# Optimization experiments

Measured on AMD Instinct MI355X. Metric: run time of the kernel, lower is better.

## Reference

```python
import jax, jax.numpy as jnp
import numpy as np

N, E, D = 50000, 300000, 64
EPS = 0.0  # eps buffer, train_eps=False


def setup_inputs() -> dict:
    key = jax.random.key(0)
    ks = jax.random.split(key, 24)
    inp = {}
    i = 0
    for d in range(3):
        inp[f"x{d}"] = jax.random.normal(ks[i], (N, D), jnp.float32); i += 1
        inp[f"up_index{d}"] = jax.random.randint(ks[i], (2, E), 0, N, jnp.int32); i += 1
        inp[f"down_index{d}"] = jax.random.randint(ks[i], (2, E), 0, N, jnp.int32); i += 1
        inp[f"up_attr{d}"] = jax.random.normal(ks[i], (E, D), jnp.float32); i += 1
        inp[f"down_attr{d}"] = jax.random.normal(ks[i], (E, D), jnp.float32); i += 1
    s2 = 1.0 / np.sqrt(2 * D)
    s1 = 1.0 / np.sqrt(D)
    inp["W_up"] = jax.random.normal(ks[i], (2 * D, D), jnp.float32) * s2; i += 1
    inp["b_up"] = jnp.zeros((D,), jnp.float32)
    inp["W_down"] = jax.random.normal(ks[i], (2 * D, D), jnp.float32) * s2; i += 1
    inp["b_down"] = jnp.zeros((D,), jnp.float32)
    inp["W1"] = jax.random.normal(ks[i], (D, D), jnp.float32) * s1; i += 1
    inp["b1"] = jnp.zeros((D,), jnp.float32)
    inp["W2"] = jax.random.normal(ks[i], (D, D), jnp.float32) * s1; i += 1
    inp["b2"] = jnp.zeros((D,), jnp.float32)
    return inp


def _level(x, up_idx, down_idx, up_attr, down_attr,
           W_up, b_up, W_down, b_down, W1, b1, W2, b2):
    # message_up: gather source feats, concat attr, MLP, scatter-add to targets
    m_up = jax.nn.relu(jnp.concatenate([x[up_idx[1]], up_attr], axis=-1) @ W_up + b_up)
    out_up = jax.ops.segment_sum(m_up, up_idx[0], num_segments=N)
    m_dn = jax.nn.relu(jnp.concatenate([x[down_idx[1]], down_attr], axis=-1) @ W_down + b_down)
    out_dn = jax.ops.segment_sum(m_dn, down_idx[0], num_segments=N)
    # out_up += (1+eps)x; out_down += (1+eps)x; update(out_up + out_down)
    h = out_up + out_dn + (2.0 * (1.0 + EPS)) * x
    return jax.nn.relu(jax.nn.relu(h @ W1 + b1) @ W2 + b2)


def reference(x0, up_index0, down_index0, up_attr0, down_attr0,
              x1, up_index1, down_index1, up_attr1, down_attr1,
              x2, up_index2, down_index2, up_attr2, down_attr2,
              W_up, b_up, W_down, b_down, W1, b1, W2, b2):
    params = (W_up, b_up, W_down, b_down, W1, b1, W2, b2)
    o0 = _level(x0, up_index0, down_index0, up_attr0, down_attr0, *params)
    o1 = _level(x1, up_index1, down_index1, up_attr1, down_attr1, *params)
    o2 = _level(x2, up_index2, down_index2, up_attr2, down_attr2, *params)
    return (o0, o1, o2)
```

## Files before the change

kernel.cpp:

```cpp
#include <hip/hip_runtime.h>
#include <hip/hip_fp16.h>

#define NN 50000
#define NE 300000
#define ETILES (NE / 16)
#define NTILES (NN / 16)

typedef _Float16 f16;
typedef _Float16 f16x4 __attribute__((ext_vector_type(4)));
typedef float f32x4 __attribute__((ext_vector_type(4)));

__device__ __forceinline__ f16x4 cvt4(float4 v) {
    f16x4 r; r.x = (f16)v.x; r.y = (f16)v.y; r.z = (f16)v.z; r.w = (f16)v.w;
    return r;
}

template<bool HALF>
__global__ void init_kernel(const float* __restrict__ x0, const float* __restrict__ x1,
                            const float* __restrict__ x2, void* __restrict__ hbase) {
    const size_t i = (size_t)blockIdx.x * 256 + threadIdx.x;
    const int lvl = (int)(i / (NN * 16));
    const size_t li = i - (size_t)lvl * (NN * 16);
    const float* xs = (lvl == 0) ? x0 : (lvl == 1) ? x1 : x2;
    float4 v = ((const float4*)xs)[li];
    if (HALF) {
        f16x4 o;
        o.x = (f16)(2.f * v.x); o.y = (f16)(2.f * v.y);
        o.z = (f16)(2.f * v.z); o.w = (f16)(2.f * v.w);
        ((f16x4*)((f16*)hbase + (size_t)lvl * NN * 64))[li] = o;
    } else {
        ((float4*)((float*)hbase + (size_t)lvl * NN * 64))[li] =
            make_float4(2.f * v.x, 2.f * v.y, 2.f * v.z, 2.f * v.w);
    }
}

template<bool HALF>
__global__ __launch_bounds__(256) void edge_kernel(
    const float* __restrict__ x, const int* __restrict__ idx,
    const float* __restrict__ attr, const float* __restrict__ W,
    const float* __restrict__ b, void* __restrict__ hv) {

    const int t    = threadIdx.x;
    const int lane = t & 63;
    const int wid  = t >> 6;
    const int lr   = lane & 15;
    const int lg   = (lane >> 4) & 3;

    f16x4 wf[8][4];
#pragma unroll
    for (int k0 = 0; k0 < 8; ++k0) {
        const int kb = k0 * 16 + 4 * lg;
#pragma unroll
        for (int n = 0; n < 4; ++n) {
            const int c = n * 16 + lr;
            f16x4 w;
            w.x = (f16)W[(kb + 0) * 64 + c];
            w.y = (f16)W[(kb + 1) * 64 + c];
            w.z = (f16)W[(kb + 2) * 64 + c];
            w.w = (f16)W[(kb + 3) * 64 + c];
            wf[k0][n] = w;
        }
    }
    float bf[4];
#pragma unroll
    for (int n = 0; n < 4; ++n) bf[n] = b[n * 16 + lr];

    const float4* x4 = (const float4*)x;
    const float4* a4 = (const float4*)attr;

    const int gw     = blockIdx.x * 4 + wid;
    const int stride = gridDim.x * 4;
    for (int tile = gw; tile < ETILES; tile += stride) {
        const int e0  = tile << 4;
        const int src = idx[NE + e0 + lr];
        int tg[4];
#pragma unroll
        for (int j = 0; j < 4; ++j) tg[j] = idx[e0 + 4 * lg + j];

        f16x4 a[8];
#pragma unroll
        for (int k0 = 0; k0 < 4; ++k0)
            a[k0] = cvt4(x4[(size_t)src * 16 + 4 * k0 + lg]);
#pragma unroll
        for (int k0 = 0; k0 < 4; ++k0)
            a[4 + k0] = cvt4(a4[(size_t)(e0 + lr) * 16 + 4 * k0 + lg]);

        f32x4 acc[4];
#pragma unroll
        for (int n = 0; n < 4; ++n) acc[n] = (f32x4){0.f, 0.f, 0.f, 0.f};
#pragma unroll
        for (int k0 = 0; k0 < 8; ++k0) {
#pragma unroll
            for (int n = 0; n < 4; ++n)
                acc[n] = __builtin_amdgcn_mfma_f32_16x16x16f16(a[k0], wf[k0][n], acc[n], 0, 0, 0);
        }

#pragma unroll
        for (int j = 0; j < 4; ++j) {
            float v[4], vn[4];
#pragma unroll
            for (int n = 0; n < 4; ++n) v[n] = fmaxf(acc[n][j] + bf[n], 0.f);
#pragma unroll
            for (int n = 0; n < 4; ++n) vn[n] = __shfl_xor(v[n], 1);
            if (HALF) {
                __half* hp = (__half*)hv + (size_t)tg[j] * 64;
                if ((lane & 1) == 0) {
                    unsafeAtomicAdd((__half2*)(hp + 0 * 16 + lr), __floats2half2_rn(v[0], vn[0]));
                    unsafeAtomicAdd((__half2*)(hp + 1 * 16 + lr), __floats2half2_rn(v[1], vn[1]));
                } else {
                    unsafeAtomicAdd((__half2*)(hp + 2 * 16 + lr - 1), __floats2half2_rn(vn[2], v[2]));
                    unsafeAtomicAdd((__half2*)(hp + 3 * 16 + lr - 1), __floats2half2_rn(vn[3], v[3]));
                }
            } else {
                float* hp = (float*)hv + (size_t)tg[j] * 64;
#pragma unroll
                for (int n = 0; n < 4; ++n)
                    unsafeAtomicAdd(hp + n * 16 + lr, v[n]);
            }
        }
    }
}

template<bool HALF>
__global__ __launch_bounds__(256) void node_kernel(
    const void* __restrict__ hbase, float* __restrict__ outb,
    const float* __restrict__ W1, const float* __restrict__ b1,
    const float* __restrict__ W2, const float* __restrict__ b2) {

    __shared__ f16 Y[4][16 * 72];

    const int t    = threadIdx.x;
    const int lane = t & 63;
    const int wid  = t >> 6;
    const int lr   = lane & 15;
    const int lg   = (lane >> 4) & 3;

    f16x4 w1f[4][4], w2f[4][4];
#pragma unroll
    for (int k0 = 0; k0 < 4; ++k0) {
        const int kb = k0 * 16 + 4 * lg;
#pragma unroll
        for (int n = 0; n < 4; ++n) {
            const int c = n * 16 + lr;
            f16x4 w;
            w.x = (f16)W1[(kb + 0) * 64 + c];
            w.y = (f16)W1[(kb + 1) * 64 + c];
            w.z = (f16)W1[(kb + 2) * 64 + c];
            w.w = (f16)W1[(kb + 3) * 64 + c];
            w1f[k0][n] = w;
            w.x = (f16)W2[(kb + 0) * 64 + c];
            w.y = (f16)W2[(kb + 1) * 64 + c];
            w.z = (f16)W2[(kb + 2) * 64 + c];
            w.w = (f16)W2[(kb + 3) * 64 + c];
            w2f[k0][n] = w;
        }
    }
    float b1f[4], b2f[4];
#pragma unroll
    for (int n = 0; n < 4; ++n) {
        b1f[n] = b1[n * 16 + lr];
        b2f[n] = b2[n * 16 + lr];
    }

    const int gw     = blockIdx.x * 4 + wid;
    const int stride = gridDim.x * 4;
    for (int tile = gw; tile < 3 * NTILES; tile += stride) {
        const int lvl = tile / NTILES;
        const int n0  = (tile - lvl * NTILES) << 4;
        float* out = outb + (size_t)lvl * NN * 64;

        f16x4 a[4];
        if (HALF) {
            const f16* h16 = (const f16*)hbase + (size_t)lvl * NN * 64;
#pragma unroll
            for (int k0 = 0; k0 < 4; ++k0)
                a[k0] = *(const f16x4*)&h16[(size_t)(n0 + lr) * 64 + k0 * 16 + 4 * lg];
        } else {
            const float4* h4 = (const float4*)((const float*)hbase + (size_t)lvl * NN * 64);
#pragma unroll
            for (int k0 = 0; k0 < 4; ++k0)
                a[k0] = cvt4(h4[(size_t)(n0 + lr) * 16 + 4 * k0 + lg]);
        }

        f32x4 acc[4];
#pragma unroll
        for (int n = 0; n < 4; ++n) acc[n] = (f32x4){0.f, 0.f, 0.f, 0.f};
#pragma unroll
        for (int k0 = 0; k0 < 4; ++k0)
#pragma unroll
            for (int n = 0; n < 4; ++n)
                acc[n] = __builtin_amdgcn_mfma_f32_16x16x16f16(a[k0], w1f[k0][n], acc[n], 0, 0, 0);

#pragma unroll
        for (int n = 0; n < 4; ++n)
#pragma unroll
            for (int j = 0; j < 4; ++j) {
                float v = acc[n][j] + b1f[n];
                v = v > 0.f ? v : 0.f;
                Y[wid][(4 * lg + j) * 72 + n * 16 + lr] = (f16)v;
            }

        f16x4 a2[4];
#pragma unroll
        for (int k0 = 0; k0 < 4; ++k0)
            a2[k0] = *(const f16x4*)&Y[wid][lr * 72 + k0 * 16 + 4 * lg];

        f32x4 acc2[4];
#pragma unroll
        for (int n = 0; n < 4; ++n) acc2[n] = (f32x4){0.f, 0.f, 0.f, 0.f};
#pragma unroll
        for (int k0 = 0; k0 < 4; ++k0)
#pragma unroll
            for (int n = 0; n < 4; ++n)
                acc2[n] = __builtin_amdgcn_mfma_f32_16x16x16f16(a2[k0], w2f[k0][n], acc2[n], 0, 0, 0);

#pragma unroll
        for (int n = 0; n < 4; ++n)
#pragma unroll
            for (int j = 0; j < 4; ++j) {
                float v = acc2[n][j] + b2f[n];
                v = v > 0.f ? v : 0.f;
                out[(size_t)(n0 + 4 * lg + j) * 64 + n * 16 + lr] = v;
            }
    }
}

extern "C" void kernel_launch(void* const* d_in, const int* in_sizes, int n_in,
                              void* d_out, int out_size, void* d_ws, size_t ws_size,
                              hipStream_t stream) {
    (void)in_sizes; (void)n_in; (void)out_size;

    const float* W_up   = (const float*)d_in[15];
    const float* b_up   = (const float*)d_in[16];
    const float* W_down = (const float*)d_in[17];
    const float* b_down = (const float*)d_in[18];
    const float* W1     = (const float*)d_in[19];
    const float* b1     = (const float*)d_in[20];
    const float* W2     = (const float*)d_in[21];
    const float* b2     = (const float*)d_in[22];

    const float* x0 = (const float*)d_in[0];
    const float* x1 = (const float*)d_in[5];
    const float* x2 = (const float*)d_in[10];

    const bool half_ok = ws_size >= (size_t)3 * NN * 64 * sizeof(__half);

    if (half_ok) {
        f16* hbase = (f16*)d_ws;
        init_kernel<true><<<9375, 256, 0, stream>>>(x0, x1, x2, hbase);
        for (int d = 0; d < 3; ++d) {
            const float* x  = (const float*)d_in[5 * d + 0];
            const int*   ui = (const int*)  d_in[5 * d + 1];
            const int*   di = (const int*)  d_in[5 * d + 2];
            const float* ua = (const float*)d_in[5 * d + 3];
            const float* da = (const float*)d_in[5 * d + 4];
            void* h = hbase + (size_t)d * NN * 64;
            edge_kernel<true><<<1024, 256, 0, stream>>>(x, ui, ua, W_up,   b_up,   h);
            edge_kernel<true><<<1024, 256, 0, stream>>>(x, di, da, W_down, b_down, h);
        }
        node_kernel<true><<<586, 256, 0, stream>>>(hbase, (float*)d_out, W1, b1, W2, b2);
    } else {
        float* hbase = (float*)d_out;
        init_kernel<false><<<9375, 256, 0, stream>>>(x0, x1, x2, hbase);
        for (int d = 0; d < 3; ++d) {
            const float* x  = (const float*)d_in[5 * d + 0];
            const int*   ui = (const int*)  d_in[5 * d + 1];
            const int*   di = (const int*)  d_in[5 * d + 2];
            const float* ua = (const float*)d_in[5 * d + 3];
            const float* da = (const float*)d_in[5 * d + 4];
            void* h = hbase + (size_t)d * NN * 64;
            edge_kernel<false><<<1024, 256, 0, stream>>>(x, ui, ua, W_up,   b_up,   h);
            edge_kernel<false><<<1024, 256, 0, stream>>>(x, di, da, W_down, b_down, h);
        }
        node_kernel<false><<<586, 256, 0, stream>>>(hbase, (float*)d_out, W1, b1, W2, b2);
    }
}
```

Measured before the change: 468.8 us.

## Merge up/down edge kernels, pretranspose weights, prefetch next edge tile

Adds a small kernel that converts W_up and W_down to f16 once and stores them transposed, so each edge wave loads its MFMA B fragments as vector loads. The up and down edge passes run in one launch using a 2D grid. Inside the loop, the indices and attributes for the next tile are software-prefetched into registers while the current tile computes. Source and target indices now come from one coalesced load spread with shuffles. This aims to hide gather and load latency and cut launch count, at the cost of more registers and an extra tiny kernel plus workspace.

```diff
diff --git a/kernel.cpp b/kernel.cpp
--- a/kernel.cpp
+++ b/kernel.cpp
@@ -34,11 +34,128 @@
     }
 }
 
-template<bool HALF>
-__global__ __launch_bounds__(256) void edge_kernel(
+__global__ void wtrans_kernel(const float* __restrict__ WU, const float* __restrict__ WD,
+                              f16* __restrict__ WtU, f16* __restrict__ WtD) {
+    const int i = blockIdx.x * 256 + threadIdx.x;
+    const int k = i >> 6, c = i & 63;
+    WtU[c * 128 + k] = (f16)WU[i];
+    WtD[c * 128 + k] = (f16)WD[i];
+}
+
+__global__ __launch_bounds__(256) void edge2_kernel(
+    const float* __restrict__ x,
+    const int* __restrict__ ui, const int* __restrict__ di,
+    const float* __restrict__ ua, const float* __restrict__ da,
+    const f16* __restrict__ WtU, const f16* __restrict__ WtD,
+    const float* __restrict__ bU, const float* __restrict__ bD,
+    __half* __restrict__ h) {
+
+    const int dir = blockIdx.y;
+    const int* __restrict__ idx   = dir ? di : ui;
+    const float* __restrict__ attr = dir ? da : ua;
+    const f16* __restrict__ Wt    = dir ? WtD : WtU;
+    const float* __restrict__ b   = dir ? bD : bU;
+
+    const int t    = threadIdx.x;
+    const int lane = t & 63;
+    const int wid  = t >> 6;
+    const int lr   = lane & 15;
+    const int lg   = (lane >> 4) & 3;
+    const int l5   = lane & 31;
+
+    f16x4 wf[8][4];
+#pragma unroll
+    for (int k0 = 0; k0 < 8; ++k0)
+#pragma unroll
+        for (int n = 0; n < 4; ++n)
+            wf[k0][n] = *(const f16x4*)&Wt[(n * 16 + lr) * 128 + k0 * 16 + 4 * lg];
+    float bf[4];
+#pragma unroll
+    for (int n = 0; n < 4; ++n) bf[n] = b[n * 16 + lr];
+
+    const float4* x4 = (const float4*)x;
+    const float4* a4 = (const float4*)attr;
+
+    const int gw     = blockIdx.x * 4 + wid;
+    const int stride = gridDim.x * 4;
+
+    int tile = gw;
+    if (tile >= ETILES) return;
+
+    int comb;
+    float4 pA[4];
+    {
+        const int e0 = tile << 4;
+        comb = idx[(l5 < 16) ? (NE + e0 + l5) : (e0 + l5 - 16)];
+#pragma unroll
+        for (int k0 = 0; k0 < 4; ++k0)
+            pA[k0] = a4[(size_t)(e0 + lr) * 16 + 4 * k0 + lg];
+    }
+
+    for (; tile < ETILES; tile += stride) {
+        const int src = __shfl(comb, lr);
+        int tg[4];
+#pragma unroll
+        for (int j = 0; j < 4; ++j) tg[j] = __shfl(comb, 16 + 4 * lg + j);
+
+        float4 gx[4];
+#pragma unroll
+        for (int k0 = 0; k0 < 4; ++k0)
+            gx[k0] = x4[(size_t)src * 16 + 4 * k0 + lg];
+
+        const int tn = tile + stride;
+        int combN = 0;
+        float4 pAn[4] = {};
+        if (tn < ETILES) {
+            const int e0n = tn << 4;
+            combN = idx[(l5 < 16) ? (NE + e0n + l5) : (e0n + l5 - 16)];
+#pragma unroll
+            for (int k0 = 0; k0 < 4; ++k0)
+                pAn[k0] = a4[(size_t)(e0n + lr) * 16 + 4 * k0 + lg];
+        }
+
+        f16x4 a[8];
+#pragma unroll
+        for (int k0 = 0; k0 < 4; ++k0) a[4 + k0] = cvt4(pA[k0]);
+#pragma unroll
+        for (int k0 = 0; k0 < 4; ++k0) a[k0] = cvt4(gx[k0]);
+
+        f32x4 acc[4];
+#pragma unroll
+        for (int n = 0; n < 4; ++n) acc[n] = (f32x4){0.f, 0.f, 0.f, 0.f};
+#pragma unroll
+        for (int k0 = 0; k0 < 8; ++k0)
+#pragma unroll
+            for (int n = 0; n < 4; ++n)
+                acc[n] = __builtin_amdgcn_mfma_f32_16x16x16f16(a[k0], wf[k0][n], acc[n], 0, 0, 0);
+
+#pragma unroll
+        for (int j = 0; j < 4; ++j) {
+            float v[4], vn[4];
+#pragma unroll
+            for (int n = 0; n < 4; ++n) v[n] = fmaxf(acc[n][j] + bf[n], 0.f);
+#pragma unroll
+            for (int n = 0; n < 4; ++n) vn[n] = __shfl_xor(v[n], 1);
+            __half* hp = h + (size_t)tg[j] * 64;
+            if ((lane & 1) == 0) {
+                unsafeAtomicAdd((__half2*)(hp + 0 * 16 + lr), __floats2half2_rn(v[0], vn[0]));
+                unsafeAtomicAdd((__half2*)(hp + 1 * 16 + lr), __floats2half2_rn(v[1], vn[1]));
+            } else {
+                unsafeAtomicAdd((__half2*)(hp + 2 * 16 + lr - 1), __floats2half2_rn(vn[2], v[2]));
+                unsafeAtomicAdd((__half2*)(hp + 3 * 16 + lr - 1), __floats2half2_rn(vn[3], v[3]));
+            }
+        }
+
+        comb = combN;
+#pragma unroll
+        for (int k0 = 0; k0 < 4; ++k0) pA[k0] = pAn[k0];
+    }
+}
+
+__global__ __launch_bounds__(256) void edge_f32_kernel(
     const float* __restrict__ x, const int* __restrict__ idx,
     const float* __restrict__ attr, const float* __restrict__ W,
-    const float* __restrict__ b, void* __restrict__ hv) {
+    const float* __restrict__ b, float* __restrict__ h) {
 
     const int t    = threadIdx.x;
     const int lane = t & 63;
@@ -89,33 +206,18 @@
 #pragma unroll
         for (int n = 0; n < 4; ++n) acc[n] = (f32x4){0.f, 0.f, 0.f, 0.f};
 #pragma unroll
-        for (int k0 = 0; k0 < 8; ++k0) {
+        for (int k0 = 0; k0 < 8; ++k0)
 #pragma unroll
             for (int n = 0; n < 4; ++n)
                 acc[n] = __builtin_amdgcn_mfma_f32_16x16x16f16(a[k0], wf[k0][n], acc[n], 0, 0, 0);
-        }
 
 #pragma unroll
         for (int j = 0; j < 4; ++j) {
-            float v[4], vn[4];
-#pragma unroll
-            for (int n = 0; n < 4; ++n) v[n] = fmaxf(acc[n][j] + bf[n], 0.f);
-#pragma unroll
-            for (int n = 0; n < 4; ++n) vn[n] = __shfl_xor(v[n], 1);
-            if (HALF) {
-                __half* hp = (__half*)hv + (size_t)tg[j] * 64;
-                if ((lane & 1) == 0) {
-                    unsafeAtomicAdd((__half2*)(hp + 0 * 16 + lr), __floats2half2_rn(v[0], vn[0]));
-                    unsafeAtomicAdd((__half2*)(hp + 1 * 16 + lr), __floats2half2_rn(v[1], vn[1]));
-                } else {
-                    unsafeAtomicAdd((__half2*)(hp + 2 * 16 + lr - 1), __floats2half2_rn(vn[2], v[2]));
-                    unsafeAtomicAdd((__half2*)(hp + 3 * 16 + lr - 1), __floats2half2_rn(vn[3], v[3]));
-                }
-            } else {
-                float* hp = (float*)hv + (size_t)tg[j] * 64;
-#pragma unroll
-                for (int n = 0; n < 4; ++n)
-                    unsafeAtomicAdd(hp + n * 16 + lr, v[n]);
+            float* hp = h + (size_t)tg[j] * 64;
+#pragma unroll
+            for (int n = 0; n < 4; ++n) {
+                float v = fmaxf(acc[n][j] + bf[n], 0.f);
+                unsafeAtomicAdd(hp + n * 16 + lr, v);
             }
         }
     }
@@ -243,10 +345,15 @@
     const float* x1 = (const float*)d_in[5];
     const float* x2 = (const float*)d_in[10];
 
-    const bool half_ok = ws_size >= (size_t)3 * NN * 64 * sizeof(__half);
+    const size_t hbytes = (size_t)3 * NN * 64 * sizeof(__half);
+    const bool half_ok = ws_size >= hbytes + 2 * 128 * 64 * sizeof(f16);
 
     if (half_ok) {
         f16* hbase = (f16*)d_ws;
+        f16* WtU = (f16*)((char*)d_ws + hbytes);
+        f16* WtD = WtU + 128 * 64;
+
+        wtrans_kernel<<<32, 256, 0, stream>>>(W_up, W_down, WtU, WtD);
         init_kernel<true><<<9375, 256, 0, stream>>>(x0, x1, x2, hbase);
         for (int d = 0; d < 3; ++d) {
             const float* x  = (const float*)d_in[5 * d + 0];
@@ -254,9 +361,9 @@
             const int*   di = (const int*)  d_in[5 * d + 2];
             const float* ua = (const float*)d_in[5 * d + 3];
             const float* da = (const float*)d_in[5 * d + 4];
-            void* h = hbase + (size_t)d * NN * 64;
-            edge_kernel<true><<<1024, 256, 0, stream>>>(x, ui, ua, W_up,   b_up,   h);
-            edge_kernel<true><<<1024, 256, 0, stream>>>(x, di, da, W_down, b_down, h);
+            __half* h = (__half*)(hbase + (size_t)d * NN * 64);
+            edge2_kernel<<<dim3(1024, 2), 256, 0, stream>>>(
+                x, ui, di, ua, da, WtU, WtD, b_up, b_down, h);
         }
         node_kernel<true><<<586, 256, 0, stream>>>(hbase, (float*)d_out, W1, b1, W2, b2);
     } else {
@@ -268,9 +375,9 @@
             const int*   di = (const int*)  d_in[5 * d + 2];
             const float* ua = (const float*)d_in[5 * d + 3];
             const float* da = (const float*)d_in[5 * d + 4];
-            void* h = hbase + (size_t)d * NN * 64;
-            edge_kernel<false><<<1024, 256, 0, stream>>>(x, ui, ua, W_up,   b_up,   h);
-            edge_kernel<false><<<1024, 256, 0, stream>>>(x, di, da, W_down, b_down, h);
+            float* h = hbase + (size_t)d * NN * 64;
+            edge_f32_kernel<<<1024, 256, 0, stream>>>(x, ui, ua, W_up,   b_up,   h);
+            edge_f32_kernel<<<1024, 256, 0, stream>>>(x, di, da, W_down, b_down, h);
         }
         node_kernel<false><<<586, 256, 0, stream>>>(hbase, (float*)d_out, W1, b1, W2, b2);
     }
```

Result: faster. 443.1 us (-5.5%).
